# Kernel tuning notes

Hardware: AMD Instinct MI355X
Metric: run time of the kernel (lower is better)

The kernel has to match this reference:

```python
import jax, jax.numpy as jnp
import numpy as np

# GeoTempScheduler default: init_temp=0.1, gamma=0.9, patience=1; at step 0 -> temp = 0.1
TEMP = 0.1

R, K, D, DLOW, B = 8, 10, 256, 10, 4096


def setup_inputs() -> dict:
    key = jax.random.key(0)
    k1, k2 = jax.random.split(key)
    x = jax.random.normal(k1, (B, D), dtype=jnp.float32)
    # reset_parameters: Us ~ N(0, 0.1/sqrt(D))
    Us = jax.random.normal(k2, (R, K, D, DLOW), dtype=jnp.float32) * (0.1 / np.sqrt(D))
    return {"x": x, "Us": Us}


def reference(x, Us):
    # encode: project data onto each (replicate, cluster) subspace basis
    # z: (r, k, B, d)
    z = jnp.einsum('bD,rkDd->rkbd', x, Us)
    # decode: x_ = z @ Us^T  -> (r, k, B, D)
    x_ = jnp.einsum('rkbd,rkDd->rkbD', z, Us)
    # l2-squared reconstruction loss, (r, k, B) -> permuted to (B, r, k)
    loss = 0.5 * jnp.sum((x_ - x) ** 2, axis=-1)
    assign_obj = jnp.transpose(loss, (2, 0, 1))  # (B, r, k)
    # set_assign uses detached objective (loss.data): temperature-scaled soft assignment
    c = jax.nn.softmax(-jax.lax.stop_gradient(assign_obj) / TEMP, axis=2)  # (B, r, k)
    # x_ * c.permute(1,2,0).unsqueeze(3), summed over clusters -> (r, B, D)
    out = jnp.einsum('rkbD,brk->rbD', x_, c)
    return out
```

## Files before the change

### kernel.cpp

```cpp
#include <hip/hip_runtime.h>
#include <math.h>

typedef unsigned short ushort_t;
typedef unsigned int uint32_tt;
typedef __attribute__((ext_vector_type(8))) short bf16x8;
typedef __attribute__((ext_vector_type(4))) float f32x4;

#define NR   8
#define NK   10
#define ND   256
#define NDL  10
#define NB   4096
#define NN   100
#define NP   112
#define NP2  128

#define WS_GP   0
#define WS_XB   32768
#define WS_U1   (32768 + 2097152)
#define WS_U2   (WS_U1 + 458752)
#define WS_NEED (WS_U2 + 524288)

__device__ __forceinline__ ushort_t f2bf(float f) {
    uint32_tt u = __float_as_uint(f);
    u = (u + 0x7FFF + ((u >> 16) & 1)) >> 16;
    return (ushort_t)u;
}

__global__ __launch_bounds__(256) void prep_kernel(const float* __restrict__ x,
                                                   const float* __restrict__ Us,
                                                   char* __restrict__ ws) {
    __shared__ float lu[ND * NDL];
    const int bid = blockIdx.x, tid = threadIdx.x;

    if (bid < 1024) {
        ushort_t* xb = (ushort_t*)(ws + WS_XB);
        int i = bid * 256 + tid;
        float4 v = ((const float4*)x)[i];
        uint32_tt p0 = (uint32_tt)f2bf(v.x) | ((uint32_tt)f2bf(v.y) << 16);
        uint32_tt p1 = (uint32_tt)f2bf(v.z) | ((uint32_tt)f2bf(v.w) << 16);
        ((uint2*)xb)[i] = make_uint2(p0, p1);
        return;
    }

    const int rk = bid - 1024;
    const int r  = rk / NK, k = rk - r * NK;
    const float* U = Us + (size_t)rk * ND * NDL;
    for (int i = tid; i < 640; i += 256)
        ((float4*)lu)[i] = ((const float4*)U)[i];
    __syncthreads();

    float* Gp = (float*)(ws + WS_GP);
    if (tid < NDL * NDL) {
        int d1 = tid / NDL, d2 = tid - d1 * NDL;
        float acc = 0.f;
        #pragma unroll 8
        for (int Di = 0; Di < ND; ++Di)
            acc += lu[Di * NDL + d1] * lu[Di * NDL + d2];
        Gp[(size_t)rk * 100 + tid] = (d1 == d2 ? 10.0f : 0.0f) - 5.0f * acc;
    }

    ushort_t* u1 = (ushort_t*)(ws + WS_U1);
    for (int p = tid; p < ND * NDL; p += 256) {
        int d = p >> 8, D = p & 255;
        u1[((size_t)r * NP + k * NDL + d) * ND + D] = f2bf(lu[D * NDL + d]);
    }

    ushort_t* u2 = (ushort_t*)(ws + WS_U2);
    {
        int D = tid;
        uint32_tt* dst = (uint32_tt*)(u2 + ((size_t)r * ND + D) * NP2 + k * NDL);
        const float* src = lu + D * NDL;
        #pragma unroll
        for (int j = 0; j < 5; ++j)
            dst[j] = (uint32_tt)f2bf(src[2 * j]) | ((uint32_tt)f2bf(src[2 * j + 1]) << 16);
    }

    if (k == NK - 1) {
        for (int p = tid; p < 12 * ND; p += 256) {
            int n = p >> 8, D = p & 255;
            u1[((size_t)r * NP + 100 + n) * ND + D] = 0;
        }
        uint32_tt* u2u = (uint32_tt*)u2;
        #pragma unroll
        for (int j = 0; j < 14; ++j)
            u2u[((size_t)r * ND + tid) * (NP2 / 2) + 50 + j] = 0;
    }
}

__global__ __launch_bounds__(256, 2) void ksub_mfma6(const char* __restrict__ ws,
                                                     float* __restrict__ out) {
    __shared__ __align__(16) char smem[37280];
    float*    zbuf = (float*)smem;
    ushort_t* wTb  = (ushort_t*)smem;
    float*    ot   = (float*)smem;
    float*    gp   = (float*)(smem + 33280);

    const int tid  = threadIdx.x;
    const int w    = tid >> 6;
    const int lane = tid & 63;
    const int c    = lane & 15;
    const int q    = lane >> 4;
    const int bid  = blockIdx.x;
    const int xcd  = bid & 7;
    const int idx  = bid >> 3;
    const int r    = idx & 7;
    const int b0   = (xcd * 16 + (idx >> 3)) * 32;
    const int bloc = (w & 1) * 16 + c;
    const int pair = w >> 1;

    const ushort_t* xb  = (const ushort_t*)(ws + WS_XB) + (size_t)(b0 + bloc) * ND + q * 8;
    const ushort_t* u1g = (const ushort_t*)(ws + WS_U1) + (size_t)r * NP * ND + c * ND + q * 8;
    const ushort_t* u2g = (const ushort_t*)(ws + WS_U2) + (size_t)r * ND * NP2 + c * NP2 + q * 8;
    const float*    gpg = (const float*)(ws + WS_GP) + (size_t)r * 1000;

    for (int i = tid; i < 1000; i += 256) gp[i] = gpg[i];

    bf16x8 xfr[8];
    #pragma unroll
    for (int Dc = 0; Dc < 8; ++Dc)
        xfr[Dc] = *(const bf16x8*)(xb + Dc * 32);

    f32x4 acc1[4];
    #pragma unroll
    for (int t = 0; t < 4; ++t) acc1[t] = (f32x4){0.f, 0.f, 0.f, 0.f};

    #pragma unroll
    for (int Dc = 0; Dc < 8; ++Dc) {
        bf16x8 a[4];
        #pragma unroll
        for (int tt = 0; tt < 4; ++tt) {
            int t = pair * 4 + tt;
            if (t < 7)
                a[tt] = *(const bf16x8*)(u1g + t * 16 * ND + Dc * 32);
        }
        #pragma unroll
        for (int tt = 0; tt < 4; ++tt) {
            int t = pair * 4 + tt;
            if (t < 7)
                acc1[tt] = __builtin_amdgcn_mfma_f32_16x16x32_bf16(a[tt], xfr[Dc], acc1[tt], 0, 0, 0);
        }
    }

    const int Dbase = pair * 128;
    bf16x8 a3[8];
    #pragma unroll
    for (int jj = 0; jj < 8; ++jj)
        a3[jj] = *(const bf16x8*)(u2g + (size_t)(Dbase + jj * 16) * NP2);

    #pragma unroll
    for (int tt = 0; tt < 4; ++tt) {
        int t = pair * 4 + tt;
        if (t < 7) {
            #pragma unroll
            for (int rg = 0; rg < 4; ++rg) {
                int n = t * 16 + q * 4 + rg;
                if (n < NN) zbuf[bloc * 100 + n] = acc1[tt][rg];
            }
        }
    }
    __syncthreads();

    const int bsm = tid >> 3;
    const int kq  = tid & 7;
    float zk[2][10], ee[2];
    {
        const float* zr = zbuf + bsm * 100;
        float L[2];
        #pragma unroll
        for (int jj = 0; jj < 2; ++jj) {
            int k = kq + 8 * jj;
            L[jj] = -1e30f;
            if (k < NK) {
                #pragma unroll
                for (int d = 0; d < 10; ++d) zk[jj][d] = zr[k * 10 + d];
                const float* g = gp + k * 100;
                float acc = 0.f;
                #pragma unroll
                for (int d1 = 0; d1 < 10; ++d1) {
                    float t2 = 0.f;
                    #pragma unroll
                    for (int d2 = 0; d2 < 10; ++d2) t2 += g[d1 * 10 + d2] * zk[jj][d2];
                    acc += t2 * zk[jj][d1];
                }
                L[jj] = acc;
            }
        }
        float m = fmaxf(L[0], L[1]);
        m = fmaxf(m, __shfl_xor(m, 1));
        m = fmaxf(m, __shfl_xor(m, 2));
        m = fmaxf(m, __shfl_xor(m, 4));
        float s = 0.f;
        #pragma unroll
        for (int jj = 0; jj < 2; ++jj) {
            ee[jj] = (kq + 8 * jj < NK) ? __expf(L[jj] - m) : 0.f;
            s += ee[jj];
        }
        s += __shfl_xor(s, 1);
        s += __shfl_xor(s, 2);
        s += __shfl_xor(s, 4);
        float inv = 1.0f / s;
        #pragma unroll
        for (int jj = 0; jj < 2; ++jj) ee[jj] *= inv;
    }
    __syncthreads();

    #pragma unroll
    for (int jj = 0; jj < 2; ++jj) {
        int k = kq + 8 * jj;
        if (k < NK) {
            #pragma unroll
            for (int d = 0; d < 10; ++d)
                wTb[bsm * 136 + k * 10 + d] = f2bf(ee[jj] * zk[jj][d]);
        }
    }
    {
        int row = tid >> 4, p = tid & 15;
        if (row < 32 && p < 14) ((uint32_tt*)wTb)[row * 68 + 50 + p] = 0;
        row = (tid + 256) >> 4;
        if (row < 32 && p < 14) ((uint32_tt*)wTb)[row * 68 + 50 + p] = 0;
    }
    __syncthreads();

    f32x4 acc3[8];
    #pragma unroll
    for (int t = 0; t < 8; ++t) acc3[t] = (f32x4){0.f, 0.f, 0.f, 0.f};

    #pragma unroll
    for (int nc = 0; nc < 4; ++nc) {
        bf16x8 bfr = *(const bf16x8*)(wTb + bloc * 136 + nc * 32 + q * 8);
        bf16x8 a[8];
        if (nc == 0) {
            #pragma unroll
            for (int jj = 0; jj < 8; ++jj) a[jj] = a3[jj];
        } else {
            #pragma unroll
            for (int jj = 0; jj < 8; ++jj)
                a[jj] = *(const bf16x8*)(u2g + (size_t)(Dbase + jj * 16) * NP2 + nc * 32);
        }
        #pragma unroll
        for (int jj = 0; jj < 8; ++jj)
            acc3[jj] = __builtin_amdgcn_mfma_f32_16x16x32_bf16(a[jj], bfr, acc3[jj], 0, 0, 0);
    }

    __syncthreads();
    #pragma unroll
    for (int jj = 0; jj < 8; ++jj)
        *(f32x4*)(ot + bloc * 260 + Dbase + jj * 16 + q * 4) = acc3[jj];
    __syncthreads();
    const size_t orow = (size_t)r * NB + b0;
    #pragma unroll
    for (int i = 0; i < 8; ++i) {
        int g4 = i * 256 + tid;
        int b  = g4 >> 6;
        int c4 = g4 & 63;
        f32x4 v = *(const f32x4*)(ot + b * 260 + c4 * 4);
        *(f32x4*)(out + (orow + b) * ND + c4 * 4) = v;
    }
}

#define XS_S 68
#define US_S 132
#define ZB_S 104
#define WT_S 68
#define U2_S 68
#define OFF_WT 0
#define OFF_SH 6800
#define OFF_GP 13600
#define SMEM_F 14600

__global__ __launch_bounds__(128) void gram_kernel(const float* __restrict__ Us,
                                                   float* __restrict__ Gp) {
    int rk = blockIdx.x;
    const float* U = Us + (size_t)rk * ND * NDL;
    __shared__ float u[ND * NDL];
    for (int i = threadIdx.x; i < ND * NDL; i += blockDim.x) u[i] = U[i];
    __syncthreads();
    int e = threadIdx.x;
    if (e < NDL * NDL) {
        int d1 = e / NDL, d2 = e % NDL;
        float acc = 0.f;
        #pragma unroll 8
        for (int Di = 0; Di < ND; ++Di)
            acc += u[Di * NDL + d1] * u[Di * NDL + d2];
        Gp[(size_t)rk * (NDL * NDL) + e] = (d1 == d2 ? 10.0f : 0.0f) - 5.0f * acc;
    }
}

__global__ __launch_bounds__(256, 2) void ksub_fused(const float* __restrict__ x,
                                                     const float* __restrict__ Us,
                                                     const float* __restrict__ Gp,
                                                     float* __restrict__ out) {
    __shared__ float smemf[SMEM_F];
    float* wT   = smemf + OFF_WT;
    float* xsf  = smemf + OFF_SH;
    float* usf  = smemf + OFF_SH + 2176;
    float* zbuf = smemf + OFF_SH;
    float* u2   = smemf + OFF_SH;
    float* gp   = smemf + OFF_GP;

    const int tid = threadIdx.x;
    const int r   = blockIdx.y;
    const int b0  = blockIdx.x * 64;

    for (int i = tid; i < NK * NDL * NDL; i += 256)
        gp[i] = Gp[(size_t)r * (NK * NDL * NDL) + i];

    const int nt = tid & 15;
    const int bt = tid >> 4;
    float acc[4][8];
    #pragma unroll
    for (int j = 0; j < 4; ++j)
        #pragma unroll
        for (int i = 0; i < 8; ++i) acc[j][i] = 0.f;

    for (int cch = 0; cch < 8; ++cch) {
        __syncthreads();
        for (int i = tid; i < 512; i += 256) {
            int b = i >> 3, f = i & 7;
            float4 v = ((const float4*)(x + (size_t)(b0 + b) * ND))[cch * 8 + f];
            float* dst = xsf + (f * 4) * XS_S + b;
            dst[0] = v.x; dst[XS_S] = v.y; dst[2 * XS_S] = v.z; dst[3 * XS_S] = v.w;
        }
        for (int p = tid; p < 320; p += 256) {
            int k = p >> 5, Dl = p & 31;
            const float* g = Us + ((size_t)((r * NK + k) * ND) + cch * 32 + Dl) * NDL;
            float* dst = usf + Dl * US_S + k * NDL;
            #pragma unroll
            for (int d = 0; d < 10; ++d) dst[d] = g[d];
        }
        __syncthreads();
        #pragma unroll 4
        for (int Dl = 0; Dl < 32; ++Dl) {
            float4 xv = *(const float4*)(xsf + Dl * XS_S + bt * 4);
            float4 ua = *(const float4*)(usf + Dl * US_S + nt * 8);
            float4 ub = *(const float4*)(usf + Dl * US_S + nt * 8 + 4);
            float xa[4] = {xv.x, xv.y, xv.z, xv.w};
            float uu[8] = {ua.x, ua.y, ua.z, ua.w, ub.x, ub.y, ub.z, ub.w};
            #pragma unroll
            for (int j = 0; j < 4; ++j)
                #pragma unroll
                for (int i = 0; i < 8; ++i) acc[j][i] += xa[j] * uu[i];
        }
    }
    __syncthreads();
    if (nt < 12) {
        #pragma unroll
        for (int j = 0; j < 4; ++j) {
            float* zp = zbuf + (bt * 4 + j) * ZB_S + nt * 8;
            *(float4*)(zp)     = make_float4(acc[j][0], acc[j][1], acc[j][2], acc[j][3]);
            *(float4*)(zp + 4) = make_float4(acc[j][4], acc[j][5], acc[j][6], acc[j][7]);
        }
    } else if (nt == 12) {
        #pragma unroll
        for (int j = 0; j < 4; ++j) {
            float* zp = zbuf + (bt * 4 + j) * ZB_S + 96;
            *(float4*)(zp) = make_float4(acc[j][0], acc[j][1], acc[j][2], acc[j][3]);
        }
    }
    __syncthreads();
    if (tid < 64) {
        const int b_l = tid;
        const float* zrow = zbuf + b_l * ZB_S;
        float L[10];
        #pragma unroll
        for (int k = 0; k < NK; ++k) {
            float zkk[10];
            #pragma unroll
            for (int d = 0; d < 10; ++d) zkk[d] = zrow[k * 10 + d];
            const float* g = gp + k * 100;
            float a2 = 0.f;
            #pragma unroll
            for (int d1 = 0; d1 < 10; ++d1) {
                float t = 0.f;
                #pragma unroll
                for (int d2 = 0; d2 < 10; ++d2) t += g[d1 * 10 + d2] * zkk[d2];
                a2 += t * zkk[d1];
            }
            L[k] = a2;
        }
        float m = L[0];
        #pragma unroll
        for (int k = 1; k < NK; ++k) m = fmaxf(m, L[k]);
        float e[10], s = 0.f;
        #pragma unroll
        for (int k = 0; k < NK; ++k) { e[k] = __expf(L[k] - m); s += e[k]; }
        float inv = 1.0f / s;
        #pragma unroll
        for (int k = 0; k < NK; ++k) {
            float ck = e[k] * inv;
            #pragma unroll
            for (int d = 0; d < 10; ++d)
                wT[(k * 10 + d) * WT_S + b_l] = ck * zrow[k * 10 + d];
        }
    }
    const int Dt  = tid & 15;
    const int bt2 = tid >> 4;
    for (int c2 = 0; c2 < 4; ++c2) {
        __syncthreads();
        for (int p = tid; p < 640; p += 256) {
            int k = p >> 6, Dl = p & 63;
            const float* g = Us + ((size_t)((r * NK + k) * ND) + c2 * 64 + Dl) * NDL;
            float* dst = u2 + (k * NDL) * U2_S + Dl;
            #pragma unroll
            for (int d = 0; d < 10; ++d) dst[d * U2_S] = g[d];
        }
        __syncthreads();
        float o[4][4];
        #pragma unroll
        for (int j = 0; j < 4; ++j)
            #pragma unroll
            for (int i = 0; i < 4; ++i) o[j][i] = 0.f;
        #pragma unroll 4
        for (int n = 0; n < NN; ++n) {
            float4 wv = *(const float4*)(wT + n * WT_S + bt2 * 4);
            float4 uv = *(const float4*)(u2 + n * U2_S + Dt * 4);
            float wa[4] = {wv.x, wv.y, wv.z, wv.w};
            float ub[4] = {uv.x, uv.y, uv.z, uv.w};
            #pragma unroll
            for (int j = 0; j < 4; ++j)
                #pragma unroll
                for (int i = 0; i < 4; ++i) o[j][i] += wa[j] * ub[i];
        }
        #pragma unroll
        for (int j = 0; j < 4; ++j) {
            float* op = out + ((size_t)r * NB + b0 + bt2 * 4 + j) * ND + c2 * 64 + Dt * 4;
            *(float4*)op = make_float4(o[j][0], o[j][1], o[j][2], o[j][3]);
        }
    }
}

extern "C" void kernel_launch(void* const* d_in, const int* in_sizes, int n_in,
                              void* d_out, int out_size, void* d_ws, size_t ws_size,
                              hipStream_t stream) {
    const float* x  = (const float*)d_in[0];
    const float* Us = (const float*)d_in[1];
    float* out = (float*)d_out;

    if (ws_size >= (size_t)WS_NEED) {
        prep_kernel<<<dim3(1104), 256, 0, stream>>>(x, Us, (char*)d_ws);
        ksub_mfma6<<<dim3(1024), 256, 0, stream>>>((const char*)d_ws, out);
    } else {
        gram_kernel<<<dim3(NR * NK), 128, 0, stream>>>(Us, (float*)d_ws);
        ksub_fused<<<dim3(NB / 64, NR), 256, 0, stream>>>(x, Us, (float*)d_ws, out);
    }
}
```

Measured before the change: 106.0 us.

## Persist U1/U2 fragments in registers and loop four batch tiles per block

The main kernel now launches 256 blocks instead of 1024. Each block loads its replicate's U1 and U2 bf16 fragments into registers once, then loops over four 32-row batch tiles, prefetching the next tile's x fragments during the current tile. This is meant to cut repeated global loads of the basis matrices and per-block gp setup. In exchange it raises register pressure (launch bounds drop to one block per SM), reduces parallelism to 256 blocks on a 256-CU-class GPU, and removes the XCD-aware block mapping.

```diff
diff --git a/kernel.cpp b/kernel.cpp
--- a/kernel.cpp
+++ b/kernel.cpp
@@ -88,7 +88,7 @@
     }
 }
 
-__global__ __launch_bounds__(256, 2) void ksub_mfma6(const char* __restrict__ ws,
+__global__ __launch_bounds__(256, 1) void ksub_mfma7(const char* __restrict__ ws,
                                                      float* __restrict__ out) {
     __shared__ __align__(16) char smem[37280];
     float*    zbuf = (float*)smem;
@@ -102,160 +102,173 @@
     const int c    = lane & 15;
     const int q    = lane >> 4;
     const int bid  = blockIdx.x;
-    const int xcd  = bid & 7;
-    const int idx  = bid >> 3;
-    const int r    = idx & 7;
-    const int b0   = (xcd * 16 + (idx >> 3)) * 32;
+    const int r    = bid & 7;
+    const int jgrp = bid >> 3;
     const int bloc = (w & 1) * 16 + c;
     const int pair = w >> 1;
-
-    const ushort_t* xb  = (const ushort_t*)(ws + WS_XB) + (size_t)(b0 + bloc) * ND + q * 8;
+    const int Dbase = pair * 128;
+
+    const ushort_t* xbase = (const ushort_t*)(ws + WS_XB);
     const ushort_t* u1g = (const ushort_t*)(ws + WS_U1) + (size_t)r * NP * ND + c * ND + q * 8;
     const ushort_t* u2g = (const ushort_t*)(ws + WS_U2) + (size_t)r * ND * NP2 + c * NP2 + q * 8;
     const float*    gpg = (const float*)(ws + WS_GP) + (size_t)r * 1000;
 
     for (int i = tid; i < 1000; i += 256) gp[i] = gpg[i];
 
-    bf16x8 xfr[8];
-    #pragma unroll
-    for (int Dc = 0; Dc < 8; ++Dc)
-        xfr[Dc] = *(const bf16x8*)(xb + Dc * 32);
-
-    f32x4 acc1[4];
-    #pragma unroll
-    for (int t = 0; t < 4; ++t) acc1[t] = (f32x4){0.f, 0.f, 0.f, 0.f};
-
+    bf16x8 u1f[32];
     #pragma unroll
     for (int Dc = 0; Dc < 8; ++Dc) {
-        bf16x8 a[4];
         #pragma unroll
         for (int tt = 0; tt < 4; ++tt) {
             int t = pair * 4 + tt;
             if (t < 7)
-                a[tt] = *(const bf16x8*)(u1g + t * 16 * ND + Dc * 32);
-        }
+                u1f[Dc * 4 + tt] = *(const bf16x8*)(u1g + t * 16 * ND + Dc * 32);
+        }
+    }
+    bf16x8 u2f[32];
+    #pragma unroll
+    for (int nc = 0; nc < 4; ++nc) {
+        #pragma unroll
+        for (int jj = 0; jj < 8; ++jj)
+            u2f[nc * 8 + jj] = *(const bf16x8*)(u2g + (size_t)(Dbase + jj * 16) * NP2 + nc * 32);
+    }
+
+    bf16x8 xfr[8], xfrn[8];
+    {
+        const ushort_t* xb = xbase + (size_t)((jgrp * 4 + 0) * 32 + bloc) * ND + q * 8;
+        #pragma unroll
+        for (int Dc = 0; Dc < 8; ++Dc)
+            xfr[Dc] = *(const bf16x8*)(xb + Dc * 32);
+    }
+
+    for (int it = 0; it < 4; ++it) {
+        const int b0 = (jgrp * 4 + it) * 32;
+
+        if (it < 3) {
+            const ushort_t* xb = xbase + (size_t)(b0 + 32 + bloc) * ND + q * 8;
+            #pragma unroll
+            for (int Dc = 0; Dc < 8; ++Dc)
+                xfrn[Dc] = *(const bf16x8*)(xb + Dc * 32);
+        }
+
+        f32x4 acc1[4];
+        #pragma unroll
+        for (int t = 0; t < 4; ++t) acc1[t] = (f32x4){0.f, 0.f, 0.f, 0.f};
+        #pragma unroll
+        for (int Dc = 0; Dc < 8; ++Dc) {
+            #pragma unroll
+            for (int tt = 0; tt < 4; ++tt) {
+                int t = pair * 4 + tt;
+                if (t < 7)
+                    acc1[tt] = __builtin_amdgcn_mfma_f32_16x16x32_bf16(u1f[Dc * 4 + tt], xfr[Dc], acc1[tt], 0, 0, 0);
+            }
+        }
+
         #pragma unroll
         for (int tt = 0; tt < 4; ++tt) {
             int t = pair * 4 + tt;
-            if (t < 7)
-                acc1[tt] = __builtin_amdgcn_mfma_f32_16x16x32_bf16(a[tt], xfr[Dc], acc1[tt], 0, 0, 0);
-        }
-    }
-
-    const int Dbase = pair * 128;
-    bf16x8 a3[8];
-    #pragma unroll
-    for (int jj = 0; jj < 8; ++jj)
-        a3[jj] = *(const bf16x8*)(u2g + (size_t)(Dbase + jj * 16) * NP2);
-
-    #pragma unroll
-    for (int tt = 0; tt < 4; ++tt) {
-        int t = pair * 4 + tt;
-        if (t < 7) {
-            #pragma unroll
-            for (int rg = 0; rg < 4; ++rg) {
-                int n = t * 16 + q * 4 + rg;
-                if (n < NN) zbuf[bloc * 100 + n] = acc1[tt][rg];
-            }
-        }
-    }
-    __syncthreads();
-
-    const int bsm = tid >> 3;
-    const int kq  = tid & 7;
-    float zk[2][10], ee[2];
-    {
-        const float* zr = zbuf + bsm * 100;
-        float L[2];
+            if (t < 7) {
+                #pragma unroll
+                for (int rg = 0; rg < 4; ++rg) {
+                    int n = t * 16 + q * 4 + rg;
+                    if (n < NN) zbuf[bloc * 100 + n] = acc1[tt][rg];
+                }
+            }
+        }
+        __syncthreads();
+
+        const int bsm = tid >> 3;
+        const int kq  = tid & 7;
+        float zk[2][10], ee[2];
+        {
+            const float* zr = zbuf + bsm * 100;
+            float L[2];
+            #pragma unroll
+            for (int jj = 0; jj < 2; ++jj) {
+                int k = kq + 8 * jj;
+                L[jj] = -1e30f;
+                if (k < NK) {
+                    #pragma unroll
+                    for (int d = 0; d < 10; ++d) zk[jj][d] = zr[k * 10 + d];
+                    const float* g = gp + k * 100;
+                    float acc = 0.f;
+                    #pragma unroll
+                    for (int d1 = 0; d1 < 10; ++d1) {
+                        float t2 = 0.f;
+                        #pragma unroll
+                        for (int d2 = 0; d2 < 10; ++d2) t2 += g[d1 * 10 + d2] * zk[jj][d2];
+                        acc += t2 * zk[jj][d1];
+                    }
+                    L[jj] = acc;
+                }
+            }
+            float m = fmaxf(L[0], L[1]);
+            m = fmaxf(m, __shfl_xor(m, 1));
+            m = fmaxf(m, __shfl_xor(m, 2));
+            m = fmaxf(m, __shfl_xor(m, 4));
+            float s = 0.f;
+            #pragma unroll
+            for (int jj = 0; jj < 2; ++jj) {
+                ee[jj] = (kq + 8 * jj < NK) ? __expf(L[jj] - m) : 0.f;
+                s += ee[jj];
+            }
+            s += __shfl_xor(s, 1);
+            s += __shfl_xor(s, 2);
+            s += __shfl_xor(s, 4);
+            float inv = 1.0f / s;
+            #pragma unroll
+            for (int jj = 0; jj < 2; ++jj) ee[jj] *= inv;
+        }
+        __syncthreads();
+
         #pragma unroll
         for (int jj = 0; jj < 2; ++jj) {
             int k = kq + 8 * jj;
-            L[jj] = -1e30f;
             if (k < NK) {
                 #pragma unroll
-                for (int d = 0; d < 10; ++d) zk[jj][d] = zr[k * 10 + d];
-                const float* g = gp + k * 100;
-                float acc = 0.f;
-                #pragma unroll
-                for (int d1 = 0; d1 < 10; ++d1) {
-                    float t2 = 0.f;
-                    #pragma unroll
-                    for (int d2 = 0; d2 < 10; ++d2) t2 += g[d1 * 10 + d2] * zk[jj][d2];
-                    acc += t2 * zk[jj][d1];
-                }
-                L[jj] = acc;
-            }
-        }
-        float m = fmaxf(L[0], L[1]);
-        m = fmaxf(m, __shfl_xor(m, 1));
-        m = fmaxf(m, __shfl_xor(m, 2));
-        m = fmaxf(m, __shfl_xor(m, 4));
-        float s = 0.f;
-        #pragma unroll
-        for (int jj = 0; jj < 2; ++jj) {
-            ee[jj] = (kq + 8 * jj < NK) ? __expf(L[jj] - m) : 0.f;
-            s += ee[jj];
-        }
-        s += __shfl_xor(s, 1);
-        s += __shfl_xor(s, 2);
-        s += __shfl_xor(s, 4);
-        float inv = 1.0f / s;
-        #pragma unroll
-        for (int jj = 0; jj < 2; ++jj) ee[jj] *= inv;
-    }
-    __syncthreads();
-
-    #pragma unroll
-    for (int jj = 0; jj < 2; ++jj) {
-        int k = kq + 8 * jj;
-        if (k < NK) {
-            #pragma unroll
-            for (int d = 0; d < 10; ++d)
-                wTb[bsm * 136 + k * 10 + d] = f2bf(ee[jj] * zk[jj][d]);
-        }
-    }
-    {
-        int row = tid >> 4, p = tid & 15;
-        if (row < 32 && p < 14) ((uint32_tt*)wTb)[row * 68 + 50 + p] = 0;
-        row = (tid + 256) >> 4;
-        if (row < 32 && p < 14) ((uint32_tt*)wTb)[row * 68 + 50 + p] = 0;
-    }
-    __syncthreads();
-
-    f32x4 acc3[8];
-    #pragma unroll
-    for (int t = 0; t < 8; ++t) acc3[t] = (f32x4){0.f, 0.f, 0.f, 0.f};
-
-    #pragma unroll
-    for (int nc = 0; nc < 4; ++nc) {
-        bf16x8 bfr = *(const bf16x8*)(wTb + bloc * 136 + nc * 32 + q * 8);
-        bf16x8 a[8];
-        if (nc == 0) {
-            #pragma unroll
-            for (int jj = 0; jj < 8; ++jj) a[jj] = a3[jj];
-        } else {
+                for (int d = 0; d < 10; ++d)
+                    wTb[bsm * 136 + k * 10 + d] = f2bf(ee[jj] * zk[jj][d]);
+            }
+        }
+        {
+            int row = tid >> 4, p = tid & 15;
+            if (p < 14) ((uint32_tt*)wTb)[row * 68 + 50 + p] = 0;
+            row += 16;
+            if (p < 14) ((uint32_tt*)wTb)[row * 68 + 50 + p] = 0;
+        }
+        __syncthreads();
+
+        f32x4 acc3[8];
+        #pragma unroll
+        for (int t = 0; t < 8; ++t) acc3[t] = (f32x4){0.f, 0.f, 0.f, 0.f};
+        #pragma unroll
+        for (int nc = 0; nc < 4; ++nc) {
+            bf16x8 bfr = *(const bf16x8*)(wTb + bloc * 136 + nc * 32 + q * 8);
             #pragma unroll
             for (int jj = 0; jj < 8; ++jj)
-                a[jj] = *(const bf16x8*)(u2g + (size_t)(Dbase + jj * 16) * NP2 + nc * 32);
-        }
+                acc3[jj] = __builtin_amdgcn_mfma_f32_16x16x32_bf16(u2f[nc * 8 + jj], bfr, acc3[jj], 0, 0, 0);
+        }
+
+        __syncthreads();
         #pragma unroll
         for (int jj = 0; jj < 8; ++jj)
-            acc3[jj] = __builtin_amdgcn_mfma_f32_16x16x32_bf16(a[jj], bfr, acc3[jj], 0, 0, 0);
-    }
-
-    __syncthreads();
-    #pragma unroll
-    for (int jj = 0; jj < 8; ++jj)
-        *(f32x4*)(ot + bloc * 260 + Dbase + jj * 16 + q * 4) = acc3[jj];
-    __syncthreads();
-    const size_t orow = (size_t)r * NB + b0;
-    #pragma unroll
-    for (int i = 0; i < 8; ++i) {
-        int g4 = i * 256 + tid;
-        int b  = g4 >> 6;
-        int c4 = g4 & 63;
-        f32x4 v = *(const f32x4*)(ot + b * 260 + c4 * 4);
-        *(f32x4*)(out + (orow + b) * ND + c4 * 4) = v;
+            *(f32x4*)(ot + bloc * 260 + Dbase + jj * 16 + q * 4) = acc3[jj];
+        __syncthreads();
+        const size_t orow = (size_t)r * NB + b0;
+        #pragma unroll
+        for (int i = 0; i < 8; ++i) {
+            int g4 = i * 256 + tid;
+            int b  = g4 >> 6;
+            int c4 = g4 & 63;
+            f32x4 v = *(const f32x4*)(ot + b * 260 + c4 * 4);
+            *(f32x4*)(out + (orow + b) * ND + c4 * 4) = v;
+        }
+        __syncthreads();
+
+        if (it < 3) {
+            #pragma unroll
+            for (int Dc = 0; Dc < 8; ++Dc) xfr[Dc] = xfrn[Dc];
+        }
     }
 }
 
@@ -439,7 +452,7 @@
 
     if (ws_size >= (size_t)WS_NEED) {
         prep_kernel<<<dim3(1104), 256, 0, stream>>>(x, Us, (char*)d_ws);
-        ksub_mfma6<<<dim3(1024), 256, 0, stream>>>((const char*)d_ws, out);
+        ksub_mfma7<<<dim3(256), 256, 0, stream>>>((const char*)d_ws, out);
     } else {
         gram_kernel<<<dim3(NR * NK), 128, 0, stream>>>(Us, (float*)d_ws);
         ksub_fused<<<dim3(NB / 64, NR), 256, 0, stream>>>(x, Us, (float*)d_ws, out);
```

Result: no change. 106.6 us (+0.5%).
